# Performance work log

Hardware: AMD Instinct MI355X
Metric: run time of the kernel (lower is better)

Reference implementation:

```python
import jax, jax.numpy as jnp
import numpy as np

B, S, D_ENC, D_DEC, UNITS = 64, 2048, 512, 512, 512


def setup_inputs() -> dict:
    key = jax.random.key(0)
    ks = jax.random.split(key, 8)
    sc = lambda d: 1.0 / np.sqrt(d)
    return {
        "encoder_output": jax.random.normal(ks[0], (B, S, D_ENC), dtype=jnp.float32),
        "decoder_hidden": jax.random.normal(ks[1], (B, D_DEC), dtype=jnp.float32),
        "W1": jax.random.normal(ks[2], (D_ENC, UNITS), dtype=jnp.float32) * sc(D_ENC),
        "b1": jnp.zeros((UNITS,), dtype=jnp.float32),
        "W2": jax.random.normal(ks[3], (D_DEC, UNITS), dtype=jnp.float32) * sc(D_DEC),
        "b2": jnp.zeros((UNITS,), dtype=jnp.float32),
        "V": jax.random.normal(ks[4], (UNITS, 1), dtype=jnp.float32) * sc(UNITS),
        "bv": jnp.zeros((1,), dtype=jnp.float32),
    }


def reference(encoder_output, decoder_hidden, W1, b1, W2, b2, V, bv):
    # score = V(tanh(W1(enc) + W2(dec)[:, None, :]))  -> [B, S, 1]
    h_enc = jnp.einsum("bsd,du->bsu", encoder_output, W1) + b1   # [B,S,U]
    h_dec = decoder_hidden @ W2 + b2                              # [B,U]
    score = jnp.tanh(h_enc + h_dec[:, None, :]) @ V + bv          # [B,S,1]
    attn = jax.nn.softmax(score, axis=1)                          # softmax over seq
    # context = sum_s attn * enc  -> [B, D_enc]
    return jnp.sum(attn * encoder_output, axis=1)
```

## Files before the change

### kernel.cpp

```cpp
#include <hip/hip_runtime.h>
#include <hip/hip_bf16.h>

#define B_ 64
#define S_ 2048
#define D_ 512
#define ROWS 64

typedef __attribute__((ext_vector_type(8))) short bf16x8;
typedef __attribute__((ext_vector_type(4))) float f32x4;

__device__ inline short f2bf(float f) {
    __hip_bfloat16 h = __float2bfloat16(f);
    return __builtin_bit_cast(short, h);
}
__device__ inline float bf2f(short s) {
    return __uint_as_float(((unsigned)(unsigned short)s) << 16);
}
__device__ inline float fast_tanh(float x) {
    float xc = fminf(fmaxf(x, -15.f), 15.f);
    float t = __expf(2.f * xc);
    return (t - 1.f) * __builtin_amdgcn_rcpf(t + 1.f);
}

__global__ __launch_bounds__(128)
void hdec_kernel(const float* __restrict__ dec, const float* __restrict__ W2,
                 const float* __restrict__ b1, const float* __restrict__ b2,
                 float* __restrict__ hdec)
{
    int b = blockIdx.x >> 2;
    int u = (blockIdx.x & 3) * 128 + threadIdx.x;
    __shared__ float ds[512];
    for (int i = threadIdx.x; i < 512; i += 128) ds[i] = dec[b * 512 + i];
    __syncthreads();
    float acc = b1[u] + b2[u];
    const float* wp = W2 + u;
    #pragma unroll 8
    for (int k = 0; k < 512; ++k)
        acc = fmaf(ds[k], wp[(size_t)k * 512], acc);
    hdec[b * 512 + u] = acc;
}

__global__ void w1t_kernel(const float* __restrict__ W1, short* __restrict__ W1T)
{
    __shared__ float tile[64][65];
    int d0 = blockIdx.x * 64;
    int u0 = blockIdx.y * 64;
    int tx = threadIdx.x & 63;
    int ty = threadIdx.x >> 6;
    #pragma unroll
    for (int i = 0; i < 16; ++i) {
        int d = ty + i * 4;
        tile[d][tx] = W1[(size_t)(d0 + d) * 512 + u0 + tx];
    }
    __syncthreads();
    #pragma unroll
    for (int i = 0; i < 16; ++i) {
        int u = ty + i * 4;
        W1T[(size_t)(u0 + u) * 512 + d0 + tx] = f2bf(tile[tx][u]);
    }
}

__global__ __launch_bounds__(256, 2)
void attn_main(const float* __restrict__ enc, const short* __restrict__ W1T,
               const float* __restrict__ hdec, const float* __restrict__ Vv,
               float* __restrict__ partials)
{
    const int blk = blockIdx.x;
    const int b = blk >> 5;
    const int chunk = blk & 31;
    const int tid = threadIdx.x;
    const int w = tid >> 6;
    const int l = tid & 63;
    const int lc = l & 15;
    const int lg = l >> 4;

    __shared__ short enc_s[ROWS * 512];
    __shared__ float s_sc[4][64];
    __shared__ float s_p[64];
    __shared__ float s_ml[2];
    __shared__ float s_ctx[4][512];

    const float* encB = enc + ((size_t)b * S_ + chunk * ROWS) * D_;

    #pragma unroll
    for (int i = 0; i < 16; ++i) {
        int e = i * 2048 + tid * 8;
        f32x4 p0 = *(const f32x4*)(encB + e);
        f32x4 p1 = *(const f32x4*)(encB + e + 4);
        bf16x8 v;
        v[0] = f2bf(p0[0]); v[1] = f2bf(p0[1]); v[2] = f2bf(p0[2]); v[3] = f2bf(p0[3]);
        v[4] = f2bf(p1[0]); v[5] = f2bf(p1[1]); v[6] = f2bf(p1[2]); v[7] = f2bf(p1[3]);
        int row = e >> 9;
        int byte = (e * 2) ^ ((row & 7) << 4);
        *(bf16x8*)((char*)enc_s + byte) = v;
    }
    __syncthreads();

    float sacc[4][4];
    #pragma unroll
    for (int g = 0; g < 4; ++g)
        #pragma unroll
        for (int r = 0; r < 4; ++r) sacc[g][r] = 0.f;

    for (int np = 0; np < 4; ++np) {
        f32x4 acc[4][2] = {};
        #pragma unroll 4
        for (int kk = 0; kk < 16; ++kk) {
            bf16x8 a[4], bb[2];
            #pragma unroll
            for (int g = 0; g < 4; ++g) {
                int row = g * 16 + lc;
                int byte = (row * 1024 + (kk * 32 + lg * 8) * 2) ^ ((lc & 7) << 4);
                a[g] = *(const bf16x8*)((const char*)enc_s + byte);
            }
            #pragma unroll
            for (int nn = 0; nn < 2; ++nn) {
                int n = w * 8 + np * 2 + nn;
                bb[nn] = *(const bf16x8*)(W1T + (size_t)(n * 16 + lc) * 512 + kk * 32 + lg * 8);
            }
            #pragma unroll
            for (int g = 0; g < 4; ++g) {
                acc[g][0] = __builtin_amdgcn_mfma_f32_16x16x32_bf16(a[g], bb[0], acc[g][0], 0, 0, 0);
                acc[g][1] = __builtin_amdgcn_mfma_f32_16x16x32_bf16(a[g], bb[1], acc[g][1], 0, 0, 0);
            }
        }
        #pragma unroll
        for (int nn = 0; nn < 2; ++nn) {
            int u = (w * 8 + np * 2 + nn) * 16 + lc;
            float hd = hdec[b * 512 + u];
            float vv = Vv[u];
            #pragma unroll
            for (int g = 0; g < 4; ++g)
                #pragma unroll
                for (int r = 0; r < 4; ++r)
                    sacc[g][r] += fast_tanh(acc[g][nn][r] + hd) * vv;
        }
    }

    #pragma unroll
    for (int g = 0; g < 4; ++g) {
        #pragma unroll
        for (int r = 0; r < 4; ++r) {
            float v = sacc[g][r];
            v += __shfl_xor(v, 1);
            v += __shfl_xor(v, 2);
            v += __shfl_xor(v, 4);
            v += __shfl_xor(v, 8);
            if (lc == 0) s_sc[w][g * 16 + lg * 4 + r] = v;
        }
    }
    __syncthreads();
    if (w == 0) {
        float x = s_sc[0][l] + s_sc[1][l] + s_sc[2][l] + s_sc[3][l];
        float mx = x;
        #pragma unroll
        for (int o = 32; o >= 1; o >>= 1) mx = fmaxf(mx, __shfl_xor(mx, o));
        float p = __expf(x - mx);
        float ps = p;
        #pragma unroll
        for (int o = 32; o >= 1; o >>= 1) ps += __shfl_xor(ps, o);
        s_p[l] = p;
        if (l == 0) { s_ml[0] = mx; s_ml[1] = ps; }
    }
    __syncthreads();

    float c8[8] = {0.f, 0.f, 0.f, 0.f, 0.f, 0.f, 0.f, 0.f};
    #pragma unroll
    for (int rr = 0; rr < 16; ++rr) {
        int row = w * 16 + rr;
        int byte = (row * 1024 + l * 16) ^ ((row & 7) << 4);
        bf16x8 ev = *(const bf16x8*)((const char*)enc_s + byte);
        float p = s_p[row];
        #pragma unroll
        for (int j = 0; j < 8; ++j) c8[j] = fmaf(p, bf2f(ev[j]), c8[j]);
    }
    #pragma unroll
    for (int j = 0; j < 8; ++j) s_ctx[w][l * 8 + j] = c8[j];
    __syncthreads();

    float* part = partials + (size_t)blk * 514;
    int d = tid * 2;
    part[d]     = s_ctx[0][d]     + s_ctx[1][d]     + s_ctx[2][d]     + s_ctx[3][d];
    part[d + 1] = s_ctx[0][d + 1] + s_ctx[1][d + 1] + s_ctx[2][d + 1] + s_ctx[3][d + 1];
    if (tid == 0) { part[512] = s_ml[0]; part[513] = s_ml[1]; }
}

__global__ void merge_kernel(const float* __restrict__ partials, float* __restrict__ out)
{
    int b = blockIdx.x;
    int tid = threadIdx.x;
    const float* pb = partials + (size_t)b * 32 * 514;
    float M = -1e30f;
    #pragma unroll
    for (int i = 0; i < 32; ++i) M = fmaxf(M, pb[i * 514 + 512]);
    float sc[32]; float L = 0.f;
    #pragma unroll
    for (int i = 0; i < 32; ++i) {
        sc[i] = __expf(pb[i * 514 + 512] - M);
        L += pb[i * 514 + 513] * sc[i];
    }
    float inv = 1.0f / L;
    int d = tid * 2;
    #pragma unroll
    for (int t = 0; t < 2; ++t) {
        float acc = 0.f;
        #pragma unroll
        for (int i = 0; i < 32; ++i) acc += pb[i * 514 + d + t] * sc[i];
        out[b * 512 + d + t] = acc * inv;
    }
}

extern "C" void kernel_launch(void* const* d_in, const int* in_sizes, int n_in,
                              void* d_out, int out_size, void* d_ws, size_t ws_size,
                              hipStream_t stream)
{
    const float* enc = (const float*)d_in[0];
    const float* dec = (const float*)d_in[1];
    const float* W1  = (const float*)d_in[2];
    const float* b1  = (const float*)d_in[3];
    const float* W2  = (const float*)d_in[4];
    const float* b2  = (const float*)d_in[5];
    const float* V   = (const float*)d_in[6];
    float* out = (float*)d_out;

    char* ws = (char*)d_ws;
    float* hdec     = (float*)ws;
    short* W1T      = (short*)(ws + 64 * 512 * 4);
    float* partials = (float*)(ws + 64 * 512 * 4 + 512 * 512 * 2);

    hipLaunchKernelGGL(hdec_kernel, dim3(256), dim3(128), 0, stream, dec, W2, b1, b2, hdec);
    hipLaunchKernelGGL(w1t_kernel, dim3(8, 8), dim3(256), 0, stream, W1, W1T);
    hipLaunchKernelGGL(attn_main, dim3(2048), dim3(256), 0, stream, enc, W1T, hdec, V, partials);
    hipLaunchKernelGGL(merge_kernel, dim3(64), dim3(256), 0, stream, partials, out);
}
```

Before: 525.1 us.

## Software-pipeline MFMA loads, widen N tile, and reduce context via shuffles

The score GEMM loop now handles four N-tiles per pass instead of two, so each A fragment loaded from LDS feeds more MFMAs. A fragments are prefetched one k-step ahead and W1T fragments two k-steps ahead from global memory, which is meant to hide load latency behind the MFMAs. The context reduction now splits D across waves and sums rows with cross-lane shuffles, which removes the s_ctx shared buffer and one __syncthreads. In exchange, register pressure rises (16 accumulators plus the prefetch buffers), and this could hurt occupancy under launch_bounds(256,2).

```diff
diff --git a/kernel.cpp b/kernel.cpp
--- a/kernel.cpp
+++ b/kernel.cpp
@@ -78,7 +78,6 @@
     __shared__ float s_sc[4][64];
     __shared__ float s_p[64];
     __shared__ float s_ml[2];
-    __shared__ float s_ctx[4][512];
 
     const float* encB = enc + ((size_t)b * S_ + chunk * ROWS) * D_;
 
@@ -102,31 +101,65 @@
         #pragma unroll
         for (int r = 0; r < 4; ++r) sacc[g][r] = 0.f;
 
-    for (int np = 0; np < 4; ++np) {
-        f32x4 acc[4][2] = {};
-        #pragma unroll 4
+    const char* encs_c = (const char*)enc_s;
+    const int swz = (lc & 7) << 4;
+
+    #pragma unroll
+    for (int np = 0; np < 2; ++np) {
+        f32x4 acc[4][4];
+        #pragma unroll
+        for (int g = 0; g < 4; ++g)
+            #pragma unroll
+            for (int nn = 0; nn < 4; ++nn) acc[g][nn] = f32x4{0.f, 0.f, 0.f, 0.f};
+
+        const short* wb = W1T + (size_t)(w * 128 + np * 64 + lc) * 512 + lg * 8;
+
+        bf16x8 a_c[4], a_n[4];
+        bf16x8 b0[4], b1v[4], b2v[4];
+
+        #pragma unroll
+        for (int nn = 0; nn < 4; ++nn) {
+            b0[nn]  = *(const bf16x8*)(wb + (size_t)nn * 16 * 512);
+            b1v[nn] = *(const bf16x8*)(wb + (size_t)nn * 16 * 512 + 32);
+        }
+        #pragma unroll
+        for (int g = 0; g < 4; ++g) {
+            int row = g * 16 + lc;
+            a_c[g] = *(const bf16x8*)(encs_c + ((row * 1024 + lg * 16) ^ swz));
+        }
+
+        #pragma unroll
         for (int kk = 0; kk < 16; ++kk) {
-            bf16x8 a[4], bb[2];
+            if (kk < 15) {
+                #pragma unroll
+                for (int g = 0; g < 4; ++g) {
+                    int row = g * 16 + lc;
+                    a_n[g] = *(const bf16x8*)(encs_c + ((row * 1024 + (kk + 1) * 64 + lg * 16) ^ swz));
+                }
+            }
+            if (kk < 14) {
+                #pragma unroll
+                for (int nn = 0; nn < 4; ++nn)
+                    b2v[nn] = *(const bf16x8*)(wb + (size_t)nn * 16 * 512 + (kk + 2) * 32);
+            }
             #pragma unroll
             for (int g = 0; g < 4; ++g) {
-                int row = g * 16 + lc;
-                int byte = (row * 1024 + (kk * 32 + lg * 8) * 2) ^ ((lc & 7) << 4);
-                a[g] = *(const bf16x8*)((const char*)enc_s + byte);
-            }
-            #pragma unroll
-            for (int nn = 0; nn < 2; ++nn) {
-                int n = w * 8 + np * 2 + nn;
-                bb[nn] = *(const bf16x8*)(W1T + (size_t)(n * 16 + lc) * 512 + kk * 32 + lg * 8);
-            }
-            #pragma unroll
-            for (int g = 0; g < 4; ++g) {
-                acc[g][0] = __builtin_amdgcn_mfma_f32_16x16x32_bf16(a[g], bb[0], acc[g][0], 0, 0, 0);
-                acc[g][1] = __builtin_amdgcn_mfma_f32_16x16x32_bf16(a[g], bb[1], acc[g][1], 0, 0, 0);
-            }
-        }
-        #pragma unroll
-        for (int nn = 0; nn < 2; ++nn) {
-            int u = (w * 8 + np * 2 + nn) * 16 + lc;
+                acc[g][0] = __builtin_amdgcn_mfma_f32_16x16x32_bf16(a_c[g], b0[0], acc[g][0], 0, 0, 0);
+                acc[g][1] = __builtin_amdgcn_mfma_f32_16x16x32_bf16(a_c[g], b0[1], acc[g][1], 0, 0, 0);
+                acc[g][2] = __builtin_amdgcn_mfma_f32_16x16x32_bf16(a_c[g], b0[2], acc[g][2], 0, 0, 0);
+                acc[g][3] = __builtin_amdgcn_mfma_f32_16x16x32_bf16(a_c[g], b0[3], acc[g][3], 0, 0, 0);
+            }
+            #pragma unroll
+            for (int i = 0; i < 4; ++i) {
+                a_c[i] = a_n[i];
+                b0[i] = b1v[i];
+                b1v[i] = b2v[i];
+            }
+        }
+
+        #pragma unroll
+        for (int nn = 0; nn < 4; ++nn) {
+            int u = (w * 8 + np * 4 + nn) * 16 + lc;
             float hd = hdec[b * 512 + u];
             float vv = Vv[u];
             #pragma unroll
@@ -164,25 +197,32 @@
     }
     __syncthreads();
 
-    float c8[8] = {0.f, 0.f, 0.f, 0.f, 0.f, 0.f, 0.f, 0.f};
-    #pragma unroll
-    for (int rr = 0; rr < 16; ++rr) {
-        int row = w * 16 + rr;
-        int byte = (row * 1024 + l * 16) ^ ((row & 7) << 4);
-        bf16x8 ev = *(const bf16x8*)((const char*)enc_s + byte);
-        float p = s_p[row];
-        #pragma unroll
-        for (int j = 0; j < 8; ++j) c8[j] = fmaf(p, bf2f(ev[j]), c8[j]);
-    }
-    #pragma unroll
-    for (int j = 0; j < 8; ++j) s_ctx[w][l * 8 + j] = c8[j];
-    __syncthreads();
-
-    float* part = partials + (size_t)blk * 514;
-    int d = tid * 2;
-    part[d]     = s_ctx[0][d]     + s_ctx[1][d]     + s_ctx[2][d]     + s_ctx[3][d];
-    part[d + 1] = s_ctx[0][d + 1] + s_ctx[1][d + 1] + s_ctx[2][d + 1] + s_ctx[3][d + 1];
-    if (tid == 0) { part[512] = s_ml[0]; part[513] = s_ml[1]; }
+    {
+        const int dblk = l & 15;
+        const int rgrp = l >> 4;
+        const int dbyte = w * 256 + dblk * 16;
+        float c8[8] = {0.f, 0.f, 0.f, 0.f, 0.f, 0.f, 0.f, 0.f};
+        #pragma unroll
+        for (int rr = 0; rr < 16; ++rr) {
+            int row = rgrp * 16 + rr;
+            bf16x8 ev = *(const bf16x8*)(encs_c + ((row * 1024 + dbyte) ^ ((row & 7) << 4)));
+            float p = s_p[row];
+            #pragma unroll
+            for (int j = 0; j < 8; ++j) c8[j] = fmaf(p, bf2f(ev[j]), c8[j]);
+        }
+        #pragma unroll
+        for (int j = 0; j < 8; ++j) {
+            c8[j] += __shfl_xor(c8[j], 16);
+            c8[j] += __shfl_xor(c8[j], 32);
+        }
+        float* part = partials + (size_t)blk * 514;
+        if (rgrp == 0) {
+            #pragma unroll
+            for (int j = 0; j < 8; ++j)
+                part[w * 128 + dblk * 8 + j] = c8[j];
+        }
+        if (tid == 0) { part[512] = s_ml[0]; part[513] = s_ml[1]; }
+    }
 }
 
 __global__ void merge_kernel(const float* __restrict__ partials, float* __restrict__ out)
```

Result: slower. 554.8 us (+5.7%).
